# Kernel tuning notes

Hardware: AMD Instinct MI355X
Metric: run time of the kernel (lower is better)

The kernel has to match this reference:

```python
import jax, jax.numpy as jnp
import numpy as np

B = 4096
IN = 1024      # input_shape * 2
H = 2048       # rnn_hidden_dim * 2
A = 64         # n_actions
A2 = A * A     # fc2 output width


def setup_inputs() -> dict:
    key = jax.random.key(0)
    ks = jax.random.split(key, 12)
    s_in = 1.0 / np.sqrt(IN)
    s_h = 1.0 / np.sqrt(H)
    return {
        "inputs": jax.random.normal(ks[0], (B, IN), jnp.float32),
        "hidden_state": jax.random.normal(ks[1], (B, H), jnp.float32),
        # fc1: Linear(IN -> H)
        "W1": jax.random.uniform(ks[2], (H, IN), jnp.float32, -s_in, s_in),
        "b1": jax.random.uniform(ks[3], (H,), jnp.float32, -s_in, s_in),
        # GRUCell(H -> H), gate order r, z, n
        "Wih": jax.random.uniform(ks[4], (3 * H, H), jnp.float32, -s_h, s_h),
        "Whh": jax.random.uniform(ks[5], (3 * H, H), jnp.float32, -s_h, s_h),
        "bih": jax.random.uniform(ks[6], (3 * H,), jnp.float32, -s_h, s_h),
        "bhh": jax.random.uniform(ks[7], (3 * H,), jnp.float32, -s_h, s_h),
        # fc2: Linear(H -> A^2)
        "W2": jax.random.uniform(ks[8], (A2, H), jnp.float32, -s_h, s_h),
        "b2": jax.random.uniform(ks[9], (A2,), jnp.float32, -s_h, s_h),
    }


# Static gather indices for the vectorized __decode_combined_output.
# Row 2i, col j: max over q[i, j : j+A]  (contiguous window)
_IDX1 = np.arange(A)[:, None] + np.arange(A)[None, :]              # [A, A]
# Row 2i+1, col j: max over q[i, k-1] for k in range(j, A^2, A);
# at j=0 the index k-1 = -1 wraps to the last element (torch semantics).
_IDX2 = (np.arange(A)[:, None] + np.arange(A)[None, :] * A - 1) % A2  # [A, A]


def reference(inputs, hidden_state, W1, b1, Wih, Whh, bih, bhh, W2, b2):
    x = jax.nn.relu(inputs @ W1.T + b1)                 # [B, H]
    h_in = hidden_state.reshape(-1, H)
    gi = x @ Wih.T + bih                                # [B, 3H]
    gh = h_in @ Whh.T + bhh                             # [B, 3H]
    ir, iz, inn = jnp.split(gi, 3, axis=1)
    hr, hz, hn = jnp.split(gh, 3, axis=1)
    r = jax.nn.sigmoid(ir + hr)
    z = jax.nn.sigmoid(iz + hz)
    n = jnp.tanh(inn + r * hn)
    h = (1.0 - z) * n + z * h_in                        # [B, H]
    q = h @ W2.T + b2                                   # [B, A^2]
    q1 = jnp.max(q[:, _IDX1], axis=-1)                  # [B, A]
    q2 = jnp.max(q[:, _IDX2], axis=-1)                  # [B, A]
    out = jnp.stack([q1, q2], axis=1).reshape(-1, A)    # interleaved [2B, A]
    return out, h
```

## Files before the change

### kernel.cpp

```cpp
#include <hip/hip_runtime.h>
#include <stdint.h>

typedef unsigned short u16;
typedef __bf16 bf16x8 __attribute__((ext_vector_type(8)));
typedef float f32x4 __attribute__((ext_vector_type(4)));
typedef u16 u16x8 __attribute__((ext_vector_type(8)));

__device__ __forceinline__ float b2f(u16 v) {
    union { float f; unsigned int u; } x; x.u = ((unsigned int)v) << 16; return x.f;
}
__device__ __forceinline__ u16 f2b(float f) {
    union { float f; unsigned int u; } x; x.f = f;
    unsigned int r = x.u + 0x7fff + ((x.u >> 16) & 1);
    return (u16)(r >> 16);
}

__device__ __forceinline__ void gll16(const void* g, void* l) {
    __builtin_amdgcn_global_load_lds(
        (const __attribute__((address_space(1))) void*)g,
        (__attribute__((address_space(3))) void*)l,
        16, 0, 0);
}

__device__ __forceinline__ bf16x8 pack8(float4 f0, float4 f1) {
    union { float4 f; uint4 u; } a, b;
    a.f = f0; b.f = f1;
    const unsigned sel = 0x07060302u;
    union { unsigned u[4]; bf16x8 v; } r;
    r.u[0] = __builtin_amdgcn_perm(a.u.y + 0x8000u, a.u.x + 0x8000u, sel);
    r.u[1] = __builtin_amdgcn_perm(a.u.w + 0x8000u, a.u.z + 0x8000u, sel);
    r.u[2] = __builtin_amdgcn_perm(b.u.y + 0x8000u, b.u.x + 0x8000u, sel);
    r.u[3] = __builtin_amdgcn_perm(b.u.w + 0x8000u, b.u.z + 0x8000u, sel);
    return r.v;
}

__global__ __launch_bounds__(256) void cvt_kernel(
    const float* __restrict__ s, u16* __restrict__ d)
{
    const size_t i = ((size_t)blockIdx.x * 256 + threadIdx.x) * 8;
    float4 f0 = *(const float4*)(s + i);
    float4 f1 = *(const float4*)(s + i + 4);
    union { bf16x8 v; u16x8 u; } r;
    r.v = pack8(f0, f1);
    *(u16x8*)(d + i) = r.u;
}


#define FBAR() do { asm volatile("" ::: "memory"); \
                    __builtin_amdgcn_s_barrier();  \
                    asm volatile("" ::: "memory"); } while (0)
#define WAIT_LGKM0() asm volatile("s_waitcnt lgkmcnt(0)" ::: "memory")
#define WAIT_VM6()   asm volatile("s_waitcnt vmcnt(6)" ::: "memory")
#define WAIT_VM0()   asm volatile("s_waitcnt vmcnt(0)" ::: "memory")

__device__ __forceinline__ void stage_half(
    const u16* __restrict__ Mp, int rowBase, int K, int k0,
    u16* region, int t, int w)
{
#pragma unroll
    for (int it = 0; it < 2; ++it) {
        const int phys = it * 512 + t;
        const int r = phys >> 3;
        const int c = (phys & 7) ^ (r & 7);
        gll16(Mp + (size_t)(rowBase + r) * K + (k0 + c * 8),
              (char*)region + (it * 512 + w * 64) * 16);
    }
}

__device__ __forceinline__ void ld_a(const u16* region, int ra, int g0,
                                     bf16x8 (&out)[4][2])
{
#pragma unroll
    for (int mi = 0; mi < 4; ++mi)
#pragma unroll
        for (int s = 0; s < 2; ++s) {
            const int lr = mi * 32 + ra;
            out[mi][s] = *(const bf16x8*)((const char*)region +
                         (lr * 8 + ((s * 4 + g0) ^ (lr & 7))) * 16);
        }
}

__device__ __forceinline__ void ld_b(const u16* region, int rb, int g0,
                                     bf16x8 (&out)[2][2])
{
#pragma unroll
    for (int ni = 0; ni < 2; ++ni)
#pragma unroll
        for (int s = 0; s < 2; ++s) {
            const int lr = ni * 64 + rb;
            out[ni][s] = *(const bf16x8*)((const char*)region +
                         (lr * 8 + ((s * 4 + g0) ^ (lr & 7))) * 16);
        }
}

template <int MO, int NO>
__device__ __forceinline__ void mfma_quad(const bf16x8 (&af)[4][2],
                                          const bf16x8 (&bf)[2][2],
                                          f32x4 (&acc)[8][4])
{
    __builtin_amdgcn_s_setprio(1);
#pragma unroll
    for (int mi = 0; mi < 4; ++mi)
#pragma unroll
        for (int ni = 0; ni < 2; ++ni)
#pragma unroll
            for (int s = 0; s < 2; ++s)
                acc[MO + mi][NO + ni] = __builtin_amdgcn_mfma_f32_16x16x32_bf16(
                    af[mi][s], bf[ni][s], acc[MO + mi][NO + ni], 0, 0, 0);
    __builtin_amdgcn_s_setprio(0);
}

template <bool RELU>
__device__ __forceinline__ void gemm_body(
    const u16* __restrict__ A, const u16* __restrict__ Bw,
    const float* __restrict__ bias, u16* __restrict__ C,
    int N, int K, int gy, int gx, int bid)
{
    __shared__ alignas(16) u16 L[2][4][8192];

    const int t = threadIdx.x;
    const int l = t & 63;
    const int w = t >> 6;
    const int wr = w >> 2;
    const int wc = w & 3;

    const int xcd = bid & 7, rem = bid >> 3;
    const int rrows = gy >> 1, rcols = gx >> 2;
    const int lr_ = rem / rcols, lc_ = rem % rcols;
    const int mBase = ((xcd >> 2) * rrows + lr_) * 256;
    const int nBase = ((xcd & 3) * rcols + lc_) * 256;

    const int frow = l & 15;
    const int g0 = l >> 4;
    const int ra = wr * 16 + frow;
    const int rb = wc * 16 + frow;

    f32x4 acc[8][4] = {};
    bf16x8 a0[4][2], a1[4][2], b0[2][2], b1[2][2];

    const int NI = K >> 7;

    stage_half(A,  mBase,       K, 0,  &L[0][0][0], t, w);
    stage_half(Bw, nBase,       K, 0,  &L[0][2][0], t, w);
    stage_half(Bw, nBase + 128, K, 0,  &L[0][3][0], t, w);
    stage_half(A,  mBase + 128, K, 0,  &L[0][1][0], t, w);
    stage_half(A,  mBase,       K, 64, &L[1][0][0], t, w);
    stage_half(Bw, nBase,       K, 64, &L[1][2][0], t, w);
    stage_half(Bw, nBase + 128, K, 64, &L[1][3][0], t, w);
    WAIT_VM6();
    FBAR();

    for (int i = 0; i < NI; ++i) {
        const bool nl = (i + 1 < NI);
        const int kT1 = (2 * i + 1) << 6;
        const int kT2 = (2 * i + 2) << 6;
        const int kT3 = (2 * i + 3) << 6;

        ld_a(&L[0][0][0], ra, g0, a0);
        ld_b(&L[0][2][0], rb, g0, b0);
        stage_half(A, mBase + 128, K, kT1, &L[1][1][0], t, w);
        FBAR();
        WAIT_LGKM0();
        mfma_quad<0, 0>(a0, b0, acc);
        FBAR();

        ld_b(&L[0][3][0], rb, g0, b1);
        if (nl) stage_half(A, mBase, K, kT2, &L[0][0][0], t, w);
        FBAR();
        WAIT_LGKM0();
        mfma_quad<0, 2>(a0, b1, acc);
        FBAR();

        ld_a(&L[0][1][0], ra, g0, a1);
        if (nl) stage_half(Bw, nBase, K, kT2, &L[0][2][0], t, w);
        FBAR();
        WAIT_LGKM0();
        mfma_quad<4, 0>(a1, b0, acc);
        FBAR();

        if (nl) stage_half(Bw, nBase + 128, K, kT2, &L[0][3][0], t, w);
        FBAR();
        mfma_quad<4, 2>(a1, b1, acc);
        if (nl) { WAIT_VM6(); } else { WAIT_VM0(); }
        FBAR();

        ld_a(&L[1][0][0], ra, g0, a0);
        ld_b(&L[1][2][0], rb, g0, b0);
        if (nl) stage_half(A, mBase + 128, K, kT2, &L[0][1][0], t, w);
        FBAR();
        WAIT_LGKM0();
        mfma_quad<0, 0>(a0, b0, acc);
        FBAR();

        ld_b(&L[1][3][0], rb, g0, b1);
        if (nl) stage_half(A, mBase, K, kT3, &L[1][0][0], t, w);
        FBAR();
        WAIT_LGKM0();
        mfma_quad<0, 2>(a0, b1, acc);
        FBAR();

        ld_a(&L[1][1][0], ra, g0, a1);
        if (nl) stage_half(Bw, nBase, K, kT3, &L[1][2][0], t, w);
        FBAR();
        WAIT_LGKM0();
        mfma_quad<4, 0>(a1, b0, acc);
        FBAR();

        if (nl) stage_half(Bw, nBase + 128, K, kT3, &L[1][3][0], t, w);
        FBAR();
        mfma_quad<4, 2>(a1, b1, acc);
        if (nl) { WAIT_VM6(); }
        FBAR();
    }

    const int rq = (l >> 4) * 4;
#pragma unroll
    for (int ni = 0; ni < 4; ++ni) {
        const int col = nBase + ni * 64 + wc * 16 + (l & 15);
        const float bv = bias[col];
#pragma unroll
        for (int mi = 0; mi < 8; ++mi) {
            const int row = mBase + mi * 32 + wr * 16 + rq;
#pragma unroll
            for (int i2 = 0; i2 < 4; ++i2) {
                float v = acc[mi][ni][i2] + bv;
                if (RELU) v = fmaxf(v, 0.0f);
                C[(size_t)(row + i2) * N + col] = f2b(v);
            }
        }
    }
}

template <bool RELU>
__global__ __launch_bounds__(512, 2) void gemm256(
    const u16* __restrict__ A, const u16* __restrict__ Bw,
    const float* __restrict__ bias, u16* __restrict__ C,
    int N, int K, int gy, int gx)
{
    gemm_body<RELU>(A, Bw, bias, C, N, K, gy, gx, blockIdx.x);
}

__global__ __launch_bounds__(512, 2) void mega_kernel(
    const u16* __restrict__ A, const u16* __restrict__ Bw,
    const float* __restrict__ bias, u16* __restrict__ C,
    int N, int K, int gy, int gx,
    const float* __restrict__ s0, u16* __restrict__ d0, int n0,
    const float* __restrict__ s1, u16* __restrict__ d1, int n1,
    const float* __restrict__ s2, u16* __restrict__ d2, int n2)
{
    const int gemmBlocks = gy * gx;
    const int bid = blockIdx.x;
    if (bid < gemmBlocks) {
        gemm_body<false>(A, Bw, bias, C, N, K, gy, gx, bid);
        return;
    }
    int cb = bid - gemmBlocks;
    const float* s; u16* d;
    if (cb < n0)            { s = s0; d = d0; }
    else if (cb < n0 + n1)  { cb -= n0; s = s1; d = d1; }
    else                    { cb -= n0 + n1; s = s2; d = d2; }
    const size_t i = ((size_t)cb * 512 + threadIdx.x) * 8;
    float4 f0 = *(const float4*)(s + i);
    float4 f1 = *(const float4*)(s + i + 4);
    union { bf16x8 v; u16x8 u; } r;
    r.v = pack8(f0, f1);
    *(u16x8*)(d + i) = r.u;
}

__global__ __launch_bounds__(256) void gru_kernel(
    const u16* __restrict__ gi, const u16* __restrict__ gh,
    const float* __restrict__ hprev, float* __restrict__ houtf,
    u16* __restrict__ houtb, int H)
{
    const size_t idx = ((size_t)blockIdx.x * 256 + threadIdx.x) * 8;
    const size_t b = idx / H;
    const size_t j = idx - b * H;
    const size_t g0 = b * (size_t)(3 * H) + j;

    u16x8 vir = *(const u16x8*)&gi[g0];
    u16x8 viz = *(const u16x8*)&gi[g0 + H];
    u16x8 vin = *(const u16x8*)&gi[g0 + 2 * H];
    u16x8 vhr = *(const u16x8*)&gh[g0];
    u16x8 vhz = *(const u16x8*)&gh[g0 + H];
    u16x8 vhn = *(const u16x8*)&gh[g0 + 2 * H];
    float4 hp0 = *(const float4*)&hprev[idx];
    float4 hp1 = *(const float4*)&hprev[idx + 4];
    float hp[8] = {hp0.x, hp0.y, hp0.z, hp0.w, hp1.x, hp1.y, hp1.z, hp1.w};
    float ho[8];
    u16x8 ob;
#pragma unroll
    for (int i = 0; i < 8; ++i) {
        float r = 1.f / (1.f + expf(-(b2f(vir[i]) + b2f(vhr[i]))));
        float z = 1.f / (1.f + expf(-(b2f(viz[i]) + b2f(vhz[i]))));
        float n = tanhf(b2f(vin[i]) + r * b2f(vhn[i]));
        float h = (1.f - z) * n + z * hp[i];
        ho[i] = h;
        ob[i] = f2b(h);
    }
    *(float4*)&houtf[idx]     = make_float4(ho[0], ho[1], ho[2], ho[3]);
    *(float4*)&houtf[idx + 4] = make_float4(ho[4], ho[5], ho[6], ho[7]);
    *(u16x8*)&houtb[idx] = ob;
}

__global__ __launch_bounds__(256) void decode_kernel(
    const u16* __restrict__ q, float* __restrict__ out)
{
    __shared__ float s[4096];
    const int row = blockIdx.x;
    const int t = threadIdx.x;
    const size_t base = (size_t)row * 4096;
#pragma unroll
    for (int i = 0; i < 16; ++i) {
        int j = t + i * 256;
        s[j] = b2f(q[base + j]);
    }
    __syncthreads();
    if (t < 64) {
        float m = -INFINITY;
#pragma unroll 8
        for (int k = 0; k < 64; ++k) m = fmaxf(m, s[t + k]);
        out[(size_t)(2 * row) * 64 + t] = m;
    } else if (t < 128) {
        const int rr = t - 64;
        float m = -INFINITY;
#pragma unroll 8
        for (int k = 0; k < 64; ++k) m = fmaxf(m, s[rr + 64 * k]);
        const int j = (rr + 1) & 63;
        out[(size_t)(2 * row + 1) * 64 + j] = m;
    }
}

extern "C" void kernel_launch(void* const* d_in, const int* in_sizes, int n_in,
                              void* d_out, int out_size, void* d_ws, size_t ws_size,
                              hipStream_t stream) {
    constexpr int Bn = 4096, IN = 1024, H = 2048, A = 64, A2 = A * A;
    constexpr size_t BH  = (size_t)Bn * H;
    constexpr size_t H3H = (size_t)3 * H * H;
    constexpr size_t HIN = (size_t)H * IN;
    constexpr size_t BIN = (size_t)Bn * IN;
    constexpr size_t A2H = (size_t)A2 * H;
    constexpr size_t B3H = (size_t)Bn * 3 * H;

    const float* inputs = (const float*)d_in[0];
    const float* h0     = (const float*)d_in[1];
    const float* W1     = (const float*)d_in[2];
    const float* b1     = (const float*)d_in[3];
    const float* Wih    = (const float*)d_in[4];
    const float* Whh    = (const float*)d_in[5];
    const float* bih    = (const float*)d_in[6];
    const float* bhh    = (const float*)d_in[7];
    const float* W2     = (const float*)d_in[8];
    const float* b2     = (const float*)d_in[9];

    float* out  = (float*)d_out;
    float* hout = out + (size_t)2 * Bn * A;

    u16* wsu  = (u16*)d_ws;
    u16* h0b  = wsu;
    u16* Whhb = wsu + BH;
    u16* gi   = wsu;
    u16* q    = wsu;
    u16* gh   = wsu + B3H;
    u16* Wihb = wsu + 2 * B3H;
    u16* hbf  = wsu + 2 * B3H;
    u16* W1b  = wsu + 2 * B3H + H3H;
    u16* inb  = W1b + HIN;
    u16* xb   = inb + BIN;
    u16* W2b  = xb + BH;

    dim3 blk(256);
    dim3 gblk(512);

    cvt_kernel<<<dim3(BH  / 2048), blk, 0, stream>>>(h0,  h0b);
    cvt_kernel<<<dim3(H3H / 2048), blk, 0, stream>>>(Whh, Whhb);

    mega_kernel<<<dim3(16 * 24 + 512 + 1024 + 3072), gblk, 0, stream>>>(
        h0b, Whhb, bhh, gh, 3 * H, H, 16, 24,
        W1,     W1b,  (int)(HIN / 4096),
        inputs, inb,  (int)(BIN / 4096),
        Wih,    Wihb, (int)(H3H / 4096));

    gemm256<true><<<dim3(16 * 8), gblk, 0, stream>>>(
        inb, W1b, b1, xb, H, IN, 16, 8);

    mega_kernel<<<dim3(16 * 24 + 2048), gblk, 0, stream>>>(
        xb, Wihb, bih, gi, 3 * H, H, 16, 24,
        W2, W2b, (int)(A2H / 4096),
        W2, W2b, 0,
        W2, W2b, 0);

    gru_kernel<<<dim3((Bn * H / 8) / 256), blk, 0, stream>>>(
        gi, gh, h0, hout, hbf, H);

    gemm256<false><<<dim3(16 * 16), gblk, 0, stream>>>(
        hbf, W2b, b2, q, A2, H, 16, 16);

    decode_kernel<<<dim3(Bn), blk, 0, stream>>>(q, out);
}
```

Before: 530.5 us.

## Regroup launches: fuse conversions, co-schedule x GEMM with gh GEMM, fast GRU math

Merges the h0/Whh/W1/input fp32→bf16 conversions into one launch and runs the fc1 GEMM alongside the hidden-gate GEMM and the Wih conversion in a single kernel, cutting the launch count and filling idle CUs. Shared memory moves to the kernel level so different GEMM bodies can share one buffer. The GRU kernel switches to __expf-based sigmoid and tanh, and the decode kernel loads q with 16-byte vector reads instead of scalar ones. The fast transcendentals slightly reduce accuracy.

```diff
diff --git a/kernel.cpp b/kernel.cpp
--- a/kernel.cpp
+++ b/kernel.cpp
@@ -34,15 +34,30 @@
     return r.v;
 }
 
-__global__ __launch_bounds__(256) void cvt_kernel(
-    const float* __restrict__ s, u16* __restrict__ d)
-{
-    const size_t i = ((size_t)blockIdx.x * 256 + threadIdx.x) * 8;
+__device__ __forceinline__ void cvt_body(const float* __restrict__ s,
+                                         u16* __restrict__ d, int cb)
+{
+    const size_t i = ((size_t)cb * 512 + threadIdx.x) * 8;
     float4 f0 = *(const float4*)(s + i);
     float4 f1 = *(const float4*)(s + i + 4);
     union { bf16x8 v; u16x8 u; } r;
     r.v = pack8(f0, f1);
     *(u16x8*)(d + i) = r.u;
+}
+
+__global__ __launch_bounds__(512) void cvt4_kernel(
+    const float* __restrict__ s0, u16* __restrict__ d0, int n0,
+    const float* __restrict__ s1, u16* __restrict__ d1, int n1,
+    const float* __restrict__ s2, u16* __restrict__ d2, int n2,
+    const float* __restrict__ s3, u16* __restrict__ d3, int n3)
+{
+    int cb = blockIdx.x;
+    const float* s; u16* d;
+    if (cb < n0)                    { s = s0; d = d0; }
+    else if ((cb -= n0) < n1)       { s = s1; d = d1; }
+    else if ((cb -= n1) < n2)       { s = s2; d = d2; }
+    else                            { cb -= n2; s = s3; d = d3; }
+    cvt_body(s, d, cb);
 }
 
 
@@ -52,6 +67,7 @@
 #define WAIT_LGKM0() asm volatile("s_waitcnt lgkmcnt(0)" ::: "memory")
 #define WAIT_VM6()   asm volatile("s_waitcnt vmcnt(6)" ::: "memory")
 #define WAIT_VM0()   asm volatile("s_waitcnt vmcnt(0)" ::: "memory")
+#define LREG(buf, idx) (Ls + ((buf) * 4 + (idx)) * 8192)
 
 __device__ __forceinline__ void stage_half(
     const u16* __restrict__ Mp, int rowBase, int K, int k0,
@@ -112,12 +128,11 @@
 
 template <bool RELU>
 __device__ __forceinline__ void gemm_body(
+    u16* Ls,
     const u16* __restrict__ A, const u16* __restrict__ Bw,
     const float* __restrict__ bias, u16* __restrict__ C,
     int N, int K, int gy, int gx, int bid)
 {
-    __shared__ alignas(16) u16 L[2][4][8192];
-
     const int t = threadIdx.x;
     const int l = t & 63;
     const int w = t >> 6;
@@ -140,13 +155,13 @@
 
     const int NI = K >> 7;
 
-    stage_half(A,  mBase,       K, 0,  &L[0][0][0], t, w);
-    stage_half(Bw, nBase,       K, 0,  &L[0][2][0], t, w);
-    stage_half(Bw, nBase + 128, K, 0,  &L[0][3][0], t, w);
-    stage_half(A,  mBase + 128, K, 0,  &L[0][1][0], t, w);
-    stage_half(A,  mBase,       K, 64, &L[1][0][0], t, w);
-    stage_half(Bw, nBase,       K, 64, &L[1][2][0], t, w);
-    stage_half(Bw, nBase + 128, K, 64, &L[1][3][0], t, w);
+    stage_half(A,  mBase,       K, 0,  LREG(0, 0), t, w);
+    stage_half(Bw, nBase,       K, 0,  LREG(0, 2), t, w);
+    stage_half(Bw, nBase + 128, K, 0,  LREG(0, 3), t, w);
+    stage_half(A,  mBase + 128, K, 0,  LREG(0, 1), t, w);
+    stage_half(A,  mBase,       K, 64, LREG(1, 0), t, w);
+    stage_half(Bw, nBase,       K, 64, LREG(1, 2), t, w);
+    stage_half(Bw, nBase + 128, K, 64, LREG(1, 3), t, w);
     WAIT_VM6();
     FBAR();
 
@@ -156,57 +171,57 @@
         const int kT2 = (2 * i + 2) << 6;
         const int kT3 = (2 * i + 3) << 6;
 
-        ld_a(&L[0][0][0], ra, g0, a0);
-        ld_b(&L[0][2][0], rb, g0, b0);
-        stage_half(A, mBase + 128, K, kT1, &L[1][1][0], t, w);
+        ld_a(LREG(0, 0), ra, g0, a0);
+        ld_b(LREG(0, 2), rb, g0, b0);
+        stage_half(A, mBase + 128, K, kT1, LREG(1, 1), t, w);
         FBAR();
         WAIT_LGKM0();
         mfma_quad<0, 0>(a0, b0, acc);
         FBAR();
 
-        ld_b(&L[0][3][0], rb, g0, b1);
-        if (nl) stage_half(A, mBase, K, kT2, &L[0][0][0], t, w);
+        ld_b(LREG(0, 3), rb, g0, b1);
+        if (nl) stage_half(A, mBase, K, kT2, LREG(0, 0), t, w);
         FBAR();
         WAIT_LGKM0();
         mfma_quad<0, 2>(a0, b1, acc);
         FBAR();
 
-        ld_a(&L[0][1][0], ra, g0, a1);
-        if (nl) stage_half(Bw, nBase, K, kT2, &L[0][2][0], t, w);
+        ld_a(LREG(0, 1), ra, g0, a1);
+        if (nl) stage_half(Bw, nBase, K, kT2, LREG(0, 2), t, w);
         FBAR();
         WAIT_LGKM0();
         mfma_quad<4, 0>(a1, b0, acc);
         FBAR();
 
-        if (nl) stage_half(Bw, nBase + 128, K, kT2, &L[0][3][0], t, w);
+        if (nl) stage_half(Bw, nBase + 128, K, kT2, LREG(0, 3), t, w);
         FBAR();
         mfma_quad<4, 2>(a1, b1, acc);
         if (nl) { WAIT_VM6(); } else { WAIT_VM0(); }
         FBAR();
 
-        ld_a(&L[1][0][0], ra, g0, a0);
-        ld_b(&L[1][2][0], rb, g0, b0);
-        if (nl) stage_half(A, mBase + 128, K, kT2, &L[0][1][0], t, w);
+        ld_a(LREG(1, 0), ra, g0, a0);
+        ld_b(LREG(1, 2), rb, g0, b0);
+        if (nl) stage_half(A, mBase + 128, K, kT2, LREG(0, 1), t, w);
         FBAR();
         WAIT_LGKM0();
         mfma_quad<0, 0>(a0, b0, acc);
         FBAR();
 
-        ld_b(&L[1][3][0], rb, g0, b1);
-        if (nl) stage_half(A, mBase, K, kT3, &L[1][0][0], t, w);
+        ld_b(LREG(1, 3), rb, g0, b1);
+        if (nl) stage_half(A, mBase, K, kT3, LREG(1, 0), t, w);
         FBAR();
         WAIT_LGKM0();
         mfma_quad<0, 2>(a0, b1, acc);
         FBAR();
 
-        ld_a(&L[1][1][0], ra, g0, a1);
-        if (nl) stage_half(Bw, nBase, K, kT3, &L[1][2][0], t, w);
+        ld_a(LREG(1, 1), ra, g0, a1);
+        if (nl) stage_half(Bw, nBase, K, kT3, LREG(1, 2), t, w);
         FBAR();
         WAIT_LGKM0();
         mfma_quad<4, 0>(a1, b0, acc);
         FBAR();
 
-        if (nl) stage_half(Bw, nBase + 128, K, kT3, &L[1][3][0], t, w);
+        if (nl) stage_half(Bw, nBase + 128, K, kT3, LREG(1, 3), t, w);
         FBAR();
         mfma_quad<4, 2>(a1, b1, acc);
         if (nl) { WAIT_VM6(); }
@@ -237,34 +252,51 @@
     const float* __restrict__ bias, u16* __restrict__ C,
     int N, int K, int gy, int gx)
 {
-    gemm_body<RELU>(A, Bw, bias, C, N, K, gy, gx, blockIdx.x);
-}
-
-__global__ __launch_bounds__(512, 2) void mega_kernel(
+    __shared__ alignas(16) u16 L[2 * 4 * 8192];
+    gemm_body<RELU>(L, A, Bw, bias, C, N, K, gy, gx, blockIdx.x);
+}
+
+__global__ __launch_bounds__(512, 2) void mega1_kernel(
+    const u16* __restrict__ ghA, const u16* __restrict__ ghB,
+    const float* __restrict__ ghBias, u16* __restrict__ ghC,
+    const u16* __restrict__ xA, const u16* __restrict__ xB,
+    const float* __restrict__ xBias, u16* __restrict__ xC,
+    const float* __restrict__ cs, u16* __restrict__ cd)
+{
+    __shared__ alignas(16) u16 L[2 * 4 * 8192];
+    int bid = blockIdx.x;
+    if (bid < 16 * 24) {
+        gemm_body<false>(L, ghA, ghB, ghBias, ghC, 6144, 2048, 16, 24, bid);
+        return;
+    }
+    bid -= 16 * 24;
+    if (bid < 16 * 8) {
+        gemm_body<true>(L, xA, xB, xBias, xC, 2048, 1024, 16, 8, bid);
+        return;
+    }
+    cvt_body(cs, cd, bid - 16 * 8);
+}
+
+__global__ __launch_bounds__(512, 2) void mega2_kernel(
     const u16* __restrict__ A, const u16* __restrict__ Bw,
     const float* __restrict__ bias, u16* __restrict__ C,
-    int N, int K, int gy, int gx,
-    const float* __restrict__ s0, u16* __restrict__ d0, int n0,
-    const float* __restrict__ s1, u16* __restrict__ d1, int n1,
-    const float* __restrict__ s2, u16* __restrict__ d2, int n2)
-{
-    const int gemmBlocks = gy * gx;
-    const int bid = blockIdx.x;
-    if (bid < gemmBlocks) {
-        gemm_body<false>(A, Bw, bias, C, N, K, gy, gx, bid);
+    const float* __restrict__ cs, u16* __restrict__ cd)
+{
+    __shared__ alignas(16) u16 L[2 * 4 * 8192];
+    int bid = blockIdx.x;
+    if (bid < 16 * 24) {
+        gemm_body<false>(L, A, Bw, bias, C, 6144, 2048, 16, 24, bid);
         return;
     }
-    int cb = bid - gemmBlocks;
-    const float* s; u16* d;
-    if (cb < n0)            { s = s0; d = d0; }
-    else if (cb < n0 + n1)  { cb -= n0; s = s1; d = d1; }
-    else                    { cb -= n0 + n1; s = s2; d = d2; }
-    const size_t i = ((size_t)cb * 512 + threadIdx.x) * 8;
-    float4 f0 = *(const float4*)(s + i);
-    float4 f1 = *(const float4*)(s + i + 4);
-    union { bf16x8 v; u16x8 u; } r;
-    r.v = pack8(f0, f1);
-    *(u16x8*)(d + i) = r.u;
+    cvt_body(cs, cd, bid - 16 * 24);
+}
+
+__device__ __forceinline__ float fsig(float x) {
+    return 1.f / (1.f + __expf(-x));
+}
+__device__ __forceinline__ float ftanh(float x) {
+    float t = __expf(2.f * fabsf(x));
+    return copysignf(1.f - 2.f / (t + 1.f), x);
 }
 
 __global__ __launch_bounds__(256) void gru_kernel(
@@ -290,9 +322,9 @@
     u16x8 ob;
 #pragma unroll
     for (int i = 0; i < 8; ++i) {
-        float r = 1.f / (1.f + expf(-(b2f(vir[i]) + b2f(vhr[i]))));
-        float z = 1.f / (1.f + expf(-(b2f(viz[i]) + b2f(vhz[i]))));
-        float n = tanhf(b2f(vin[i]) + r * b2f(vhn[i]));
+        float r = fsig(b2f(vir[i]) + b2f(vhr[i]));
+        float z = fsig(b2f(viz[i]) + b2f(vhz[i]));
+        float n = ftanh(b2f(vin[i]) + r * b2f(vhn[i]));
         float h = (1.f - z) * n + z * hp[i];
         ho[i] = h;
         ob[i] = f2b(h);
@@ -310,9 +342,11 @@
     const int t = threadIdx.x;
     const size_t base = (size_t)row * 4096;
 #pragma unroll
-    for (int i = 0; i < 16; ++i) {
-        int j = t + i * 256;
-        s[j] = b2f(q[base + j]);
+    for (int i = 0; i < 2; ++i) {
+        const int j = t * 8 + i * 2048;
+        u16x8 v = *(const u16x8*)&q[base + j];
+#pragma unroll
+        for (int k2 = 0; k2 < 8; ++k2) s[j + k2] = b2f(v[k2]);
     }
     __syncthreads();
     if (t < 64) {
@@ -371,28 +405,19 @@
     dim3 blk(256);
     dim3 gblk(512);
 
-    cvt_kernel<<<dim3(BH  / 2048), blk, 0, stream>>>(h0,  h0b);
-    cvt_kernel<<<dim3(H3H / 2048), blk, 0, stream>>>(Whh, Whhb);
-
-    mega_kernel<<<dim3(16 * 24 + 512 + 1024 + 3072), gblk, 0, stream>>>(
-        h0b, Whhb, bhh, gh, 3 * H, H, 16, 24,
-        W1,     W1b,  (int)(HIN / 4096),
-        inputs, inb,  (int)(BIN / 4096),
-        Wih,    Wihb, (int)(H3H / 4096));
-
-    gemm256<true><<<dim3(16 * 8), gblk, 0, stream>>>(
-        inb, W1b, b1, xb, H, IN, 16, 8);
-
-    mega_kernel<<<dim3(16 * 24 + 2048), gblk, 0, stream>>>(
-        xb, Wihb, bih, gi, 3 * H, H, 16, 24,
-        W2, W2b, (int)(A2H / 4096),
-        W2, W2b, 0,
-        W2, W2b, 0);
+    cvt4_kernel<<<dim3(2048 + 3072 + 512 + 1024), gblk, 0, stream>>>(
+        h0, h0b, 2048, Whh, Whhb, 3072, W1, W1b, 512, inputs, inb, 1024);
+
+    mega1_kernel<<<dim3(384 + 128 + 3072), gblk, 0, stream>>>(
+        h0b, Whhb, bhh, gh, inb, W1b, b1, xb, Wih, Wihb);
+
+    mega2_kernel<<<dim3(384 + 2048), gblk, 0, stream>>>(
+        xb, Wihb, bih, gi, W2, W2b);
 
     gru_kernel<<<dim3((Bn * H / 8) / 256), blk, 0, stream>>>(
         gi, gh, h0, hout, hbf, H);
 
-    gemm256<false><<<dim3(16 * 16), gblk, 0, stream>>>(
+    gemm256<false><<<dim3(256), gblk, 0, stream>>>(
         hbf, W2b, b2, q, A2, H, 16, 16);
 
     decode_kernel<<<dim3(Bn), blk, 0, stream>>>(q, out);
```

Result: faster. 502.1 us (-5.4%).
